# Kernel tuning notes

Hardware: AMD Instinct MI355X
Metric: run time of the kernel (lower is better)

Reference implementation:

```python
import jax, jax.numpy as jnp
import numpy as np

N_NODES = 50000
ALPHA = 0.1
K_ITERS = 10


def setup_inputs() -> dict:
    key = jax.random.key(0)
    ks = jax.random.split(key, 6)
    x = jax.random.normal(ks[0], (N_NODES, 256), dtype=jnp.float32)
    edge_index = jax.random.randint(ks[1], (2, 800000), 0, N_NODES, dtype=jnp.int64)
    # Glorot-ish scaled weights
    W1 = jax.random.normal(ks[2], (256, 128), dtype=jnp.float32) * (1.0 / np.sqrt(256))
    b1 = jnp.zeros((128,), dtype=jnp.float32)
    W3 = jax.random.normal(ks[3], (128, 64), dtype=jnp.float32) * (1.0 / np.sqrt(128))
    b3 = jnp.zeros((64,), dtype=jnp.float32)
    return {"x": x, "edge_index": edge_index, "W1": W1, "b1": b1, "W3": W3, "b3": b3}


def _gcn_norm(edge_index, n_nodes):
    # Add self-loops, then symmetric normalization D^{-1/2} (A+I) D^{-1/2}
    loops = jnp.arange(n_nodes, dtype=edge_index.dtype)
    src = jnp.concatenate([edge_index[0], loops])
    dst = jnp.concatenate([edge_index[1], loops])
    deg = jax.ops.segment_sum(jnp.ones_like(dst, dtype=jnp.float32), dst,
                              num_segments=n_nodes)
    dinv = jnp.where(deg > 0, jax.lax.rsqrt(deg), 0.0)
    w = dinv[src] * dinv[dst]  # [E + N]
    return src, dst, w


def _propagate(h, src, dst, w, n_nodes):
    # out[dst] += w * h[src]  (gather -> scale -> scatter-add)
    msgs = w[:, None] * h[src]
    return jax.ops.segment_sum(msgs, dst, num_segments=n_nodes)


def reference(x, edge_index, W1, b1, W3, b3):
    n = x.shape[0]
    src, dst, w = _gcn_norm(edge_index, n)

    # GCNConv 1: linear then normalized propagation
    h = _propagate(x @ W1 + b1, src, dst, w, n)

    # APPNP: K iterations of h = (1-alpha)*A_hat h + alpha*h0 (eval: no edge dropout)
    h0 = h

    def step(hc, _):
        hn = (1.0 - ALPHA) * _propagate(hc, src, dst, w, n) + ALPHA * h0
        return hn, None

    h, _ = jax.lax.scan(step, h, None, length=K_ITERS)

    # GCNConv 2
    out = _propagate(h @ W3 + b3, src, dst, w, n)
    return out
```

## Files before the change

### kernel.cpp

```cpp
#include <hip/hip_runtime.h>

#define NN 50000
#define NE 800000
#define NT (NE + NN)


__global__ void zero_deg_kernel(int* deg) {
  int v = blockIdx.x * 256 + threadIdx.x;
  if (v < NN) deg[v] = 0;
}

__global__ void count_deg_kernel(const int* __restrict__ edst, int* __restrict__ deg) {
  int i = blockIdx.x * 256 + threadIdx.x;
  if (i < NE) atomicAdd(&deg[edst[i]], 1);
}

__global__ void dinv_kernel(const int* __restrict__ deg, float* __restrict__ dinv) {
  int v = blockIdx.x * 256 + threadIdx.x;
  if (v < NN) dinv[v] = rsqrtf((float)(deg[v] + 1));
}

__global__ __launch_bounds__(1024) void scan1_kernel(const int* __restrict__ deg,
                                                     int* __restrict__ incl,
                                                     int* __restrict__ bsum) {
  __shared__ int sd[1024];
  int gid = blockIdx.x * 1024 + threadIdx.x;
  int v = (gid < NN) ? (deg[gid] + 1) : 0;
  sd[threadIdx.x] = v;
  __syncthreads();
  for (int off = 1; off < 1024; off <<= 1) {
    int t = (threadIdx.x >= off) ? sd[threadIdx.x - off] : 0;
    __syncthreads();
    sd[threadIdx.x] += t;
    __syncthreads();
  }
  if (gid < NN) incl[gid] = sd[threadIdx.x];
  if (threadIdx.x == 1023) bsum[blockIdx.x] = sd[1023];
}

__global__ void scan2_kernel(int* bsum, int nb) {
  if (threadIdx.x == 0 && blockIdx.x == 0) {
    int run = 0;
    for (int i = 0; i < nb; ++i) { int t = bsum[i]; bsum[i] = run; run += t; }
  }
}

__global__ void scan3_kernel(const int* __restrict__ deg, const int* __restrict__ incl,
                             const int* __restrict__ bsum, int* __restrict__ offs,
                             int* __restrict__ cursor) {
  int v = blockIdx.x * 256 + threadIdx.x;
  if (v >= NN) return;
  int o = bsum[v >> 10] + incl[v] - (deg[v] + 1);
  offs[v] = o;
  cursor[v] = o;
  if (v == 0) offs[NN] = NT;
}

__global__ void fill_kernel(const int* __restrict__ esrc, const int* __restrict__ edst,
                            const float* __restrict__ dinv, int* __restrict__ cursor,
                            int2* __restrict__ edges) {
  int i = blockIdx.x * 256 + threadIdx.x;
  if (i >= NT) return;
  int s, d;
  if (i < NE) { s = esrc[i]; d = edst[i]; }
  else        { s = d = i - NE; }
  int p = atomicAdd(&cursor[d], 1);
  int2 e;
  e.x = s;
  e.y = __float_as_int(dinv[s] * dinv[d]);
  edges[p] = e;
}

__global__ void rowsum_kernel(const int* __restrict__ offs, const int2* __restrict__ edges,
                              float* __restrict__ rowsum) {
  int v = blockIdx.x * 256 + threadIdx.x;
  if (v >= NN) return;
  float s = 0.f;
  int e1 = offs[v + 1];
  for (int e = offs[v]; e < e1; ++e) s += __int_as_float(edges[e].y);
  rowsum[v] = s;
}


__global__ void w13_kernel(const float* __restrict__ W1, const float* __restrict__ W3,
                           float* __restrict__ W13) {
  int idx = blockIdx.x * 256 + threadIdx.x;
  if (idx >= 256 * 64) return;
  int r = idx >> 6, c = idx & 63;
  float acc = 0.f;
  for (int k = 0; k < 128; ++k) acc += W1[r * 128 + k] * W3[k * 64 + c];
  W13[idx] = acc;
}

__global__ void b13_kernel(const float* __restrict__ b1, const float* __restrict__ W3,
                           float* __restrict__ b13) {
  int c = threadIdx.x;
  if (c >= 64) return;
  float acc = 0.f;
  for (int k = 0; k < 128; ++k) acc += b1[k] * W3[k * 64 + c];
  b13[c] = acc;
}


template <int K>
__global__ __launch_bounds__(256) void gemm64_kernel(const float* __restrict__ A,
                                                     const float* __restrict__ W,
                                                     const float* __restrict__ bias,
                                                     float* __restrict__ out, int M) {
  __shared__ float xs[32][33];
  __shared__ float ws[32][64];

  int tid = threadIdx.x;
  int tc = tid >> 4;
  int tr = tid & 15;
  int row0 = blockIdx.x * 32;

  float acc[2][4] = {};

  for (int kc = 0; kc < K; kc += 32) {
    {
      int r = tid >> 3, k4 = tid & 7;
      int row = row0 + r;
      float4 v = make_float4(0.f, 0.f, 0.f, 0.f);
      if (row < M) v = *reinterpret_cast<const float4*>(&A[(size_t)row * K + kc + k4 * 4]);
      xs[r][k4 * 4 + 0] = v.x;
      xs[r][k4 * 4 + 1] = v.y;
      xs[r][k4 * 4 + 2] = v.z;
      xs[r][k4 * 4 + 3] = v.w;
    }
    for (int i = tid; i < 512; i += 256) {
      int k = i >> 4, c4 = i & 15;
      *reinterpret_cast<float4*>(&ws[k][c4 * 4]) =
          *reinterpret_cast<const float4*>(&W[(size_t)(kc + k) * 64 + c4 * 4]);
    }
    __syncthreads();
#pragma unroll
    for (int k = 0; k < 32; ++k) {
      float x0 = xs[tr * 2 + 0][k];
      float x1 = xs[tr * 2 + 1][k];
      float4 wv = *reinterpret_cast<const float4*>(&ws[k][tc * 4]);
      acc[0][0] += x0 * wv.x; acc[0][1] += x0 * wv.y;
      acc[0][2] += x0 * wv.z; acc[0][3] += x0 * wv.w;
      acc[1][0] += x1 * wv.x; acc[1][1] += x1 * wv.y;
      acc[1][2] += x1 * wv.z; acc[1][3] += x1 * wv.w;
    }
    __syncthreads();
  }

  float4 bv = *reinterpret_cast<const float4*>(&bias[tc * 4]);
#pragma unroll
  for (int r = 0; r < 2; ++r) {
    int row = row0 + tr * 2 + r;
    if (row < M) {
      float4 o;
      o.x = acc[r][0] + bv.x;
      o.y = acc[r][1] + bv.y;
      o.z = acc[r][2] + bv.z;
      o.w = acc[r][3] + bv.w;
      *reinterpret_cast<float4*>(&out[(size_t)row * 64 + tc * 4]) = o;
    }
  }
}


template <int MODE>
__global__ __launch_bounds__(256) void prop64_kernel(const float* __restrict__ hin,
                                                     const float* __restrict__ h0,
                                                     float* __restrict__ out,
                                                     const int* __restrict__ offs,
                                                     const int2* __restrict__ edges,
                                                     const float* __restrict__ rowsum,
                                                     const float* __restrict__ b3) {
  int node = blockIdx.x * 16 + (threadIdx.x >> 4);
  if (node >= NN) return;
  int f = (threadIdx.x & 15) * 4;
  const float* __restrict__ hb = hin + f;

  int e = offs[node];
  int e1 = offs[node + 1];
  float ax = 0.f, ay = 0.f, az = 0.f, aw = 0.f;

  for (; e + 7 < e1; e += 8) {
    int2 m[8];
#pragma unroll
    for (int j = 0; j < 8; ++j) m[j] = edges[e + j];
    float4 v[8];
#pragma unroll
    for (int j = 0; j < 8; ++j)
      v[j] = *reinterpret_cast<const float4*>(hb + (size_t)m[j].x * 64);
#pragma unroll
    for (int j = 0; j < 8; ++j) {
      float wv = __int_as_float(m[j].y);
      ax += wv * v[j].x; ay += wv * v[j].y; az += wv * v[j].z; aw += wv * v[j].w;
    }
  }
  for (; e + 1 < e1; e += 2) {
    int2 m0 = edges[e], m1 = edges[e + 1];
    float4 v0 = *reinterpret_cast<const float4*>(hb + (size_t)m0.x * 64);
    float4 v1 = *reinterpret_cast<const float4*>(hb + (size_t)m1.x * 64);
    float w0 = __int_as_float(m0.y), w1 = __int_as_float(m1.y);
    ax += w0 * v0.x + w1 * v1.x;
    ay += w0 * v0.y + w1 * v1.y;
    az += w0 * v0.z + w1 * v1.z;
    aw += w0 * v0.w + w1 * v1.w;
  }
  if (e < e1) {
    int2 m = edges[e];
    float4 v = *reinterpret_cast<const float4*>(hb + (size_t)m.x * 64);
    float wv = __int_as_float(m.y);
    ax += wv * v.x; ay += wv * v.y; az += wv * v.z; aw += wv * v.w;
  }

  if (MODE == 1) {
    float4 z = *reinterpret_cast<const float4*>(&h0[(size_t)node * 64 + f]);
    ax = 0.9f * ax + 0.1f * z.x;
    ay = 0.9f * ay + 0.1f * z.y;
    az = 0.9f * az + 0.1f * z.z;
    aw = 0.9f * aw + 0.1f * z.w;
  }
  if (MODE == 2) {
    float rs = rowsum[node];
    float4 bz = *reinterpret_cast<const float4*>(&b3[f]);
    ax += rs * bz.x; ay += rs * bz.y; az += rs * bz.z; aw += rs * bz.w;
  }
  float4 o = make_float4(ax, ay, az, aw);
  *reinterpret_cast<float4*>(&out[(size_t)node * 64 + f]) = o;
}


extern "C" void kernel_launch(void* const* d_in, const int* in_sizes, int n_in,
                              void* d_out, int out_size, void* d_ws, size_t ws_size,
                              hipStream_t stream) {
  const float* x    = (const float*)d_in[0];
  const int*   eidx = (const int*)d_in[1];
  const float* W1   = (const float*)d_in[2];
  const float* b1   = (const float*)d_in[3];
  const float* W3   = (const float*)d_in[4];
  const float* b3   = (const float*)d_in[5];
  float* outp = (float*)d_out;

  const int* esrc = eidx;
  const int* edst = eidx + NE;

  char* w = (char*)d_ws;
  size_t off = 0;
  auto take = [&](size_t bytes) {
    void* p = w + off;
    off = (off + bytes + 255) & ~(size_t)255;
    return p;
  };
  int*   deg    = (int*)take(NN * 4);
  float* dinv   = (float*)take(NN * 4);
  int*   incl   = (int*)take(NN * 4);
  int*   offs   = (int*)take((NN + 1) * 4);
  int*   cursor = (int*)take(NN * 4);
  int*   bsum   = (int*)take(64 * 4);
  float* rsum   = (float*)take(NN * 4);
  float* W13    = (float*)take(256 * 64 * 4);
  float* b13    = (float*)take(64 * 4);
  int2*  edges  = (int2*)take((size_t)NT * 8);
  float* y0     = (float*)take((size_t)NN * 64 * 4);
  float* z0     = (float*)take((size_t)NN * 64 * 4);
  float* zp     = (float*)take((size_t)NN * 64 * 4);
  float* zq     = (float*)take((size_t)NN * 64 * 4);
  (void)ws_size; (void)in_sizes; (void)n_in; (void)out_size;

  const int nblkN = (NN + 255) / 256;
  const int nblkE = (NE + 255) / 256;
  const int nblkT = (NT + 255) / 256;
  const int nbScan = (NN + 1023) / 1024;

  w13_kernel<<<64, 256, 0, stream>>>(W1, W3, W13);
  b13_kernel<<<1, 64, 0, stream>>>(b1, W3, b13);

  zero_deg_kernel<<<nblkN, 256, 0, stream>>>(deg);
  count_deg_kernel<<<nblkE, 256, 0, stream>>>(edst, deg);
  dinv_kernel<<<nblkN, 256, 0, stream>>>(deg, dinv);
  scan1_kernel<<<nbScan, 1024, 0, stream>>>(deg, incl, bsum);
  scan2_kernel<<<1, 64, 0, stream>>>(bsum, nbScan);
  scan3_kernel<<<nblkN, 256, 0, stream>>>(deg, incl, bsum, offs, cursor);
  fill_kernel<<<nblkT, 256, 0, stream>>>(esrc, edst, dinv, cursor, edges);
  rowsum_kernel<<<nblkN, 256, 0, stream>>>(offs, edges, rsum);

  gemm64_kernel<256><<<(NN + 31) / 32, 256, 0, stream>>>(x, W13, b13, y0, NN);

  const int pblk = (NN + 15) / 16;

  prop64_kernel<0><<<pblk, 256, 0, stream>>>(y0, nullptr, z0, offs, edges, nullptr, nullptr);

  const float* hc = z0;
  float* bufs[2] = {zp, zq};
  for (int it = 0; it < 10; ++it) {
    float* hn = bufs[it & 1];
    prop64_kernel<1><<<pblk, 256, 0, stream>>>(hc, z0, hn, offs, edges, nullptr, nullptr);
    hc = hn;
  }

  prop64_kernel<2><<<pblk, 256, 0, stream>>>(hc, nullptr, outp, offs, edges, rsum, b3);
}
```

Before: 515.4 us.

## Pad CSR rows to multiples of 8, split SoA edges, degree-sort nodes, retile GEMM

Each CSR row is padded to a multiple of 8 with zero-weight entries, and edge sources and weights move into separate arrays. This lets the propagation loop do aligned int4/float4 loads in one branch-free 8-wide loop. Nodes are bucketed by padded degree into a permutation, so the 16 nodes in a block have similar trip counts and wave divergence drops. The GEMM tile grows to 64 rows with 4x4 register blocking and vector LDS reads. The cost is more preprocessing kernels and extra padded traffic, since padded edges still gather h[0].

```diff
diff --git a/kernel.cpp b/kernel.cpp
--- a/kernel.cpp
+++ b/kernel.cpp
@@ -2,12 +2,13 @@
 
 #define NN 50000
 #define NE 800000
-#define NT (NE + NN)
-
-
-__global__ void zero_deg_kernel(int* deg) {
+#define NTP (NE + 8 * NN)
+
+
+__global__ void zero_deg_kernel(int* deg, int* hist) {
   int v = blockIdx.x * 256 + threadIdx.x;
   if (v < NN) deg[v] = 0;
+  if (v < 16) hist[v] = 0;
 }
 
 __global__ void count_deg_kernel(const int* __restrict__ edst, int* __restrict__ deg) {
@@ -18,6 +19,10 @@
 __global__ void dinv_kernel(const int* __restrict__ deg, float* __restrict__ dinv) {
   int v = blockIdx.x * 256 + threadIdx.x;
   if (v < NN) dinv[v] = rsqrtf((float)(deg[v] + 1));
+}
+
+__device__ __forceinline__ int pdeg_of(int deg) {
+  return ((deg + 8) >> 3) << 3;
 }
 
 __global__ __launch_bounds__(1024) void scan1_kernel(const int* __restrict__ deg,
@@ -25,7 +30,7 @@
                                                      int* __restrict__ bsum) {
   __shared__ int sd[1024];
   int gid = blockIdx.x * 1024 + threadIdx.x;
-  int v = (gid < NN) ? (deg[gid] + 1) : 0;
+  int v = (gid < NN) ? pdeg_of(deg[gid]) : 0;
   sd[threadIdx.x] = v;
   __syncthreads();
   for (int off = 1; off < 1024; off <<= 1) {
@@ -50,35 +55,71 @@
                              int* __restrict__ cursor) {
   int v = blockIdx.x * 256 + threadIdx.x;
   if (v >= NN) return;
-  int o = bsum[v >> 10] + incl[v] - (deg[v] + 1);
+  int pd = pdeg_of(deg[v]);
+  int o = bsum[v >> 10] + incl[v] - pd;
   offs[v] = o;
   cursor[v] = o;
-  if (v == 0) offs[NN] = NT;
+  if (v == NN - 1) offs[NN] = o + pd;
+}
+
+__global__ void zero_csrc_kernel(int* csrc) {
+  int i = blockIdx.x * 256 + threadIdx.x;
+  if (i < NTP) csrc[i] = 0;
 }
 
 __global__ void fill_kernel(const int* __restrict__ esrc, const int* __restrict__ edst,
-                            const float* __restrict__ dinv, int* __restrict__ cursor,
-                            int2* __restrict__ edges) {
+                            int* __restrict__ cursor, int* __restrict__ csrc) {
   int i = blockIdx.x * 256 + threadIdx.x;
-  if (i >= NT) return;
+  if (i >= NE + NN) return;
   int s, d;
   if (i < NE) { s = esrc[i]; d = edst[i]; }
   else        { s = d = i - NE; }
   int p = atomicAdd(&cursor[d], 1);
-  int2 e;
-  e.x = s;
-  e.y = __float_as_int(dinv[s] * dinv[d]);
-  edges[p] = e;
-}
-
-__global__ void rowsum_kernel(const int* __restrict__ offs, const int2* __restrict__ edges,
-                              float* __restrict__ rowsum) {
+  csrc[p] = s;
+}
+
+__global__ void cwrs_kernel(const int* __restrict__ deg, const float* __restrict__ dinv,
+                            const int* __restrict__ offs, const int* __restrict__ csrc,
+                            float* __restrict__ cw, float* __restrict__ rowsum) {
   int v = blockIdx.x * 256 + threadIdx.x;
   if (v >= NN) return;
+  float dv = dinv[v];
+  int r = deg[v] + 1;
+  int e0 = offs[v], e1 = offs[v + 1];
   float s = 0.f;
-  int e1 = offs[v + 1];
-  for (int e = offs[v]; e < e1; ++e) s += __int_as_float(edges[e].y);
+  for (int e = e0; e < e1; ++e) {
+    int j = e - e0;
+    float w = 0.f;
+    if (j < r) { w = dinv[csrc[e]] * dv; s += w; }
+    cw[e] = w;
+  }
   rowsum[v] = s;
+}
+
+
+__global__ void hist_kernel(const int* __restrict__ deg, int* __restrict__ hist) {
+  int v = blockIdx.x * 256 + threadIdx.x;
+  if (v >= NN) return;
+  int b = pdeg_of(deg[v]) >> 3;
+  if (b > 15) b = 15;
+  atomicAdd(&hist[b], 1);
+}
+
+__global__ void hscan_kernel(const int* __restrict__ hist, int* __restrict__ hcur) {
+  if (threadIdx.x == 0 && blockIdx.x == 0) {
+    int run = 0;
+    for (int i = 0; i < 16; ++i) { hcur[i] = run; run += hist[i]; }
+  }
+}
+
+__global__ void permfill_kernel(const int* __restrict__ deg, int* __restrict__ hcur,
+                                int* __restrict__ perm) {
+  int v = blockIdx.x * 256 + threadIdx.x;
+  if (v >= NN) return;
+  int b = pdeg_of(deg[v]) >> 3;
+  if (b > 15) b = 15;
+  int p = atomicAdd(&hcur[b], 1);
+  perm[p] = v;
 }
 
 
@@ -107,26 +148,23 @@
                                                      const float* __restrict__ W,
                                                      const float* __restrict__ bias,
                                                      float* __restrict__ out, int M) {
-  __shared__ float xs[32][33];
+  __shared__ float xs[64][36];
   __shared__ float ws[32][64];
 
   int tid = threadIdx.x;
-  int tc = tid >> 4;
-  int tr = tid & 15;
-  int row0 = blockIdx.x * 32;
-
-  float acc[2][4] = {};
+  int tc = tid & 15;
+  int tr = tid >> 4;
+  int row0 = blockIdx.x * 64;
+
+  float acc[4][4] = {};
 
   for (int kc = 0; kc < K; kc += 32) {
-    {
-      int r = tid >> 3, k4 = tid & 7;
+    for (int i = tid; i < 512; i += 256) {
+      int r = i >> 3, k4 = i & 7;
       int row = row0 + r;
       float4 v = make_float4(0.f, 0.f, 0.f, 0.f);
       if (row < M) v = *reinterpret_cast<const float4*>(&A[(size_t)row * K + kc + k4 * 4]);
-      xs[r][k4 * 4 + 0] = v.x;
-      xs[r][k4 * 4 + 1] = v.y;
-      xs[r][k4 * 4 + 2] = v.z;
-      xs[r][k4 * 4 + 3] = v.w;
+      *reinterpret_cast<float4*>(&xs[r][k4 * 4]) = v;
     }
     for (int i = tid; i < 512; i += 256) {
       int k = i >> 4, c4 = i & 15;
@@ -135,22 +173,29 @@
     }
     __syncthreads();
 #pragma unroll
-    for (int k = 0; k < 32; ++k) {
-      float x0 = xs[tr * 2 + 0][k];
-      float x1 = xs[tr * 2 + 1][k];
-      float4 wv = *reinterpret_cast<const float4*>(&ws[k][tc * 4]);
-      acc[0][0] += x0 * wv.x; acc[0][1] += x0 * wv.y;
-      acc[0][2] += x0 * wv.z; acc[0][3] += x0 * wv.w;
-      acc[1][0] += x1 * wv.x; acc[1][1] += x1 * wv.y;
-      acc[1][2] += x1 * wv.z; acc[1][3] += x1 * wv.w;
+    for (int kk = 0; kk < 32; kk += 4) {
+      float4 xv[4], wv[4];
+#pragma unroll
+      for (int r = 0; r < 4; ++r)
+        xv[r] = *reinterpret_cast<const float4*>(&xs[tr * 4 + r][kk]);
+#pragma unroll
+      for (int q = 0; q < 4; ++q)
+        wv[q] = *reinterpret_cast<const float4*>(&ws[kk + q][tc * 4]);
+#pragma unroll
+      for (int r = 0; r < 4; ++r) {
+        acc[r][0] += xv[r].x * wv[0].x + xv[r].y * wv[1].x + xv[r].z * wv[2].x + xv[r].w * wv[3].x;
+        acc[r][1] += xv[r].x * wv[0].y + xv[r].y * wv[1].y + xv[r].z * wv[2].y + xv[r].w * wv[3].y;
+        acc[r][2] += xv[r].x * wv[0].z + xv[r].y * wv[1].z + xv[r].z * wv[2].z + xv[r].w * wv[3].z;
+        acc[r][3] += xv[r].x * wv[0].w + xv[r].y * wv[1].w + xv[r].z * wv[2].w + xv[r].w * wv[3].w;
+      }
     }
     __syncthreads();
   }
 
   float4 bv = *reinterpret_cast<const float4*>(&bias[tc * 4]);
 #pragma unroll
-  for (int r = 0; r < 2; ++r) {
-    int row = row0 + tr * 2 + r;
+  for (int r = 0; r < 4; ++r) {
+    int row = row0 + tr * 4 + r;
     if (row < M) {
       float4 o;
       o.x = acc[r][0] + bv.x;
@@ -168,11 +213,14 @@
                                                      const float* __restrict__ h0,
                                                      float* __restrict__ out,
                                                      const int* __restrict__ offs,
-                                                     const int2* __restrict__ edges,
+                                                     const int* __restrict__ csrc,
+                                                     const float* __restrict__ cw,
+                                                     const int* __restrict__ perm,
                                                      const float* __restrict__ rowsum,
                                                      const float* __restrict__ b3) {
-  int node = blockIdx.x * 16 + (threadIdx.x >> 4);
-  if (node >= NN) return;
+  int gi = blockIdx.x * 16 + (threadIdx.x >> 4);
+  if (gi >= NN) return;
+  int node = perm[gi];
   int f = (threadIdx.x & 15) * 4;
   const float* __restrict__ hb = hin + f;
 
@@ -180,35 +228,27 @@
   int e1 = offs[node + 1];
   float ax = 0.f, ay = 0.f, az = 0.f, aw = 0.f;
 
-  for (; e + 7 < e1; e += 8) {
-    int2 m[8];
-#pragma unroll
-    for (int j = 0; j < 8; ++j) m[j] = edges[e + j];
-    float4 v[8];
-#pragma unroll
-    for (int j = 0; j < 8; ++j)
-      v[j] = *reinterpret_cast<const float4*>(hb + (size_t)m[j].x * 64);
-#pragma unroll
-    for (int j = 0; j < 8; ++j) {
-      float wv = __int_as_float(m[j].y);
-      ax += wv * v[j].x; ay += wv * v[j].y; az += wv * v[j].z; aw += wv * v[j].w;
-    }
-  }
-  for (; e + 1 < e1; e += 2) {
-    int2 m0 = edges[e], m1 = edges[e + 1];
-    float4 v0 = *reinterpret_cast<const float4*>(hb + (size_t)m0.x * 64);
-    float4 v1 = *reinterpret_cast<const float4*>(hb + (size_t)m1.x * 64);
-    float w0 = __int_as_float(m0.y), w1 = __int_as_float(m1.y);
-    ax += w0 * v0.x + w1 * v1.x;
-    ay += w0 * v0.y + w1 * v1.y;
-    az += w0 * v0.z + w1 * v1.z;
-    aw += w0 * v0.w + w1 * v1.w;
-  }
-  if (e < e1) {
-    int2 m = edges[e];
-    float4 v = *reinterpret_cast<const float4*>(hb + (size_t)m.x * 64);
-    float wv = __int_as_float(m.y);
-    ax += wv * v.x; ay += wv * v.y; az += wv * v.z; aw += wv * v.w;
+  for (; e < e1; e += 8) {
+    int4 sa = *reinterpret_cast<const int4*>(csrc + e);
+    int4 sb = *reinterpret_cast<const int4*>(csrc + e + 4);
+    float4 wa = *reinterpret_cast<const float4*>(cw + e);
+    float4 wb = *reinterpret_cast<const float4*>(cw + e + 4);
+    float4 v0 = *reinterpret_cast<const float4*>(hb + (size_t)sa.x * 64);
+    float4 v1 = *reinterpret_cast<const float4*>(hb + (size_t)sa.y * 64);
+    float4 v2 = *reinterpret_cast<const float4*>(hb + (size_t)sa.z * 64);
+    float4 v3 = *reinterpret_cast<const float4*>(hb + (size_t)sa.w * 64);
+    float4 v4 = *reinterpret_cast<const float4*>(hb + (size_t)sb.x * 64);
+    float4 v5 = *reinterpret_cast<const float4*>(hb + (size_t)sb.y * 64);
+    float4 v6 = *reinterpret_cast<const float4*>(hb + (size_t)sb.z * 64);
+    float4 v7 = *reinterpret_cast<const float4*>(hb + (size_t)sb.w * 64);
+    ax += wa.x * v0.x + wa.y * v1.x + wa.z * v2.x + wa.w * v3.x
+        + wb.x * v4.x + wb.y * v5.x + wb.z * v6.x + wb.w * v7.x;
+    ay += wa.x * v0.y + wa.y * v1.y + wa.z * v2.y + wa.w * v3.y
+        + wb.x * v4.y + wb.y * v5.y + wb.z * v6.y + wb.w * v7.y;
+    az += wa.x * v0.z + wa.y * v1.z + wa.z * v2.z + wa.w * v3.z
+        + wb.x * v4.z + wb.y * v5.z + wb.z * v6.z + wb.w * v7.z;
+    aw += wa.x * v0.w + wa.y * v1.w + wa.z * v2.w + wa.w * v3.w
+        + wb.x * v4.w + wb.y * v5.w + wb.z * v6.w + wb.w * v7.w;
   }
 
   if (MODE == 1) {
@@ -255,10 +295,14 @@
   int*   offs   = (int*)take((NN + 1) * 4);
   int*   cursor = (int*)take(NN * 4);
   int*   bsum   = (int*)take(64 * 4);
+  int*   hist   = (int*)take(16 * 4);
+  int*   hcur   = (int*)take(16 * 4);
+  int*   perm   = (int*)take(NN * 4);
   float* rsum   = (float*)take(NN * 4);
   float* W13    = (float*)take(256 * 64 * 4);
   float* b13    = (float*)take(64 * 4);
-  int2*  edges  = (int2*)take((size_t)NT * 8);
+  int*   csrc   = (int*)take((size_t)NTP * 4);
+  float* cw     = (float*)take((size_t)NTP * 4);
   float* y0     = (float*)take((size_t)NN * 64 * 4);
   float* z0     = (float*)take((size_t)NN * 64 * 4);
   float* zp     = (float*)take((size_t)NN * 64 * 4);
@@ -267,34 +311,40 @@
 
   const int nblkN = (NN + 255) / 256;
   const int nblkE = (NE + 255) / 256;
-  const int nblkT = (NT + 255) / 256;
+  const int nblkF = (NE + NN + 255) / 256;
+  const int nblkP = (NTP + 255) / 256;
   const int nbScan = (NN + 1023) / 1024;
 
   w13_kernel<<<64, 256, 0, stream>>>(W1, W3, W13);
   b13_kernel<<<1, 64, 0, stream>>>(b1, W3, b13);
 
-  zero_deg_kernel<<<nblkN, 256, 0, stream>>>(deg);
+  zero_deg_kernel<<<nblkN, 256, 0, stream>>>(deg, hist);
   count_deg_kernel<<<nblkE, 256, 0, stream>>>(edst, deg);
   dinv_kernel<<<nblkN, 256, 0, stream>>>(deg, dinv);
   scan1_kernel<<<nbScan, 1024, 0, stream>>>(deg, incl, bsum);
   scan2_kernel<<<1, 64, 0, stream>>>(bsum, nbScan);
   scan3_kernel<<<nblkN, 256, 0, stream>>>(deg, incl, bsum, offs, cursor);
-  fill_kernel<<<nblkT, 256, 0, stream>>>(esrc, edst, dinv, cursor, edges);
-  rowsum_kernel<<<nblkN, 256, 0, stream>>>(offs, edges, rsum);
-
-  gemm64_kernel<256><<<(NN + 31) / 32, 256, 0, stream>>>(x, W13, b13, y0, NN);
+  zero_csrc_kernel<<<nblkP, 256, 0, stream>>>(csrc);
+  fill_kernel<<<nblkF, 256, 0, stream>>>(esrc, edst, cursor, csrc);
+  cwrs_kernel<<<nblkN, 256, 0, stream>>>(deg, dinv, offs, csrc, cw, rsum);
+
+  hist_kernel<<<nblkN, 256, 0, stream>>>(deg, hist);
+  hscan_kernel<<<1, 64, 0, stream>>>(hist, hcur);
+  permfill_kernel<<<nblkN, 256, 0, stream>>>(deg, hcur, perm);
+
+  gemm64_kernel<256><<<(NN + 63) / 64, 256, 0, stream>>>(x, W13, b13, y0, NN);
 
   const int pblk = (NN + 15) / 16;
 
-  prop64_kernel<0><<<pblk, 256, 0, stream>>>(y0, nullptr, z0, offs, edges, nullptr, nullptr);
+  prop64_kernel<0><<<pblk, 256, 0, stream>>>(y0, nullptr, z0, offs, csrc, cw, perm, nullptr, nullptr);
 
   const float* hc = z0;
   float* bufs[2] = {zp, zq};
   for (int it = 0; it < 10; ++it) {
     float* hn = bufs[it & 1];
-    prop64_kernel<1><<<pblk, 256, 0, stream>>>(hc, z0, hn, offs, edges, nullptr, nullptr);
+    prop64_kernel<1><<<pblk, 256, 0, stream>>>(hc, z0, hn, offs, csrc, cw, perm, nullptr, nullptr);
     hc = hn;
   }
 
-  prop64_kernel<2><<<pblk, 256, 0, stream>>>(hc, nullptr, outp, offs, edges, rsum, b3);
-}
+  prop64_kernel<2><<<pblk, 256, 0, stream>>>(hc, nullptr, outp, offs, csrc, cw, perm, rsum, b3);
+}
```

Result: slower. 1.304 ms (+152.9%).

## Pad CSR rows to multiples of eight and enlarge GEMM register tile

Applied to the files above, without the earlier changes.

Each node's CSR row length (degree plus self-loop) is rounded up to a multiple of eight, and the padding slots are zeroed as (src 0, weight 0) entries. The propagation loop then always processes full groups of eight, with 16-byte vector loads for the edge records and no remainder loops. The GEMM is also retiled to 64 rows per block with a 4x4 register tile and float4 shared-memory reads. Padding adds wasted gathers of node 0 plus an extra zeroing kernel, in exchange for branch-free, vectorised inner loops.

```diff
diff --git a/kernel.cpp b/kernel.cpp
--- a/kernel.cpp
+++ b/kernel.cpp
@@ -2,7 +2,7 @@
 
 #define NN 50000
 #define NE 800000
-#define NT (NE + NN)
+#define NTP (NE + 8 * NN)
 
 
 __global__ void zero_deg_kernel(int* deg) {
@@ -18,6 +18,10 @@
 __global__ void dinv_kernel(const int* __restrict__ deg, float* __restrict__ dinv) {
   int v = blockIdx.x * 256 + threadIdx.x;
   if (v < NN) dinv[v] = rsqrtf((float)(deg[v] + 1));
+}
+
+__device__ __forceinline__ int pdeg_of(int deg) {
+  return ((deg + 8) >> 3) << 3;
 }
 
 __global__ __launch_bounds__(1024) void scan1_kernel(const int* __restrict__ deg,
@@ -25,7 +29,7 @@
                                                      int* __restrict__ bsum) {
   __shared__ int sd[1024];
   int gid = blockIdx.x * 1024 + threadIdx.x;
-  int v = (gid < NN) ? (deg[gid] + 1) : 0;
+  int v = (gid < NN) ? pdeg_of(deg[gid]) : 0;
   sd[threadIdx.x] = v;
   __syncthreads();
   for (int off = 1; off < 1024; off <<= 1) {
@@ -50,17 +54,23 @@
                              int* __restrict__ cursor) {
   int v = blockIdx.x * 256 + threadIdx.x;
   if (v >= NN) return;
-  int o = bsum[v >> 10] + incl[v] - (deg[v] + 1);
+  int pd = pdeg_of(deg[v]);
+  int o = bsum[v >> 10] + incl[v] - pd;
   offs[v] = o;
   cursor[v] = o;
-  if (v == 0) offs[NN] = NT;
+  if (v == NN - 1) offs[NN] = o + pd;
+}
+
+__global__ void zero_edges_kernel(int2* edges) {
+  int i = blockIdx.x * 256 + threadIdx.x;
+  if (i < NTP) edges[i] = make_int2(0, 0);
 }
 
 __global__ void fill_kernel(const int* __restrict__ esrc, const int* __restrict__ edst,
                             const float* __restrict__ dinv, int* __restrict__ cursor,
                             int2* __restrict__ edges) {
   int i = blockIdx.x * 256 + threadIdx.x;
-  if (i >= NT) return;
+  if (i >= NE + NN) return;
   int s, d;
   if (i < NE) { s = esrc[i]; d = edst[i]; }
   else        { s = d = i - NE; }
@@ -107,26 +117,23 @@
                                                      const float* __restrict__ W,
                                                      const float* __restrict__ bias,
                                                      float* __restrict__ out, int M) {
-  __shared__ float xs[32][33];
+  __shared__ float xs[64][36];
   __shared__ float ws[32][64];
 
   int tid = threadIdx.x;
-  int tc = tid >> 4;
-  int tr = tid & 15;
-  int row0 = blockIdx.x * 32;
-
-  float acc[2][4] = {};
+  int tc = tid & 15;
+  int tr = tid >> 4;
+  int row0 = blockIdx.x * 64;
+
+  float acc[4][4] = {};
 
   for (int kc = 0; kc < K; kc += 32) {
-    {
-      int r = tid >> 3, k4 = tid & 7;
+    for (int i = tid; i < 512; i += 256) {
+      int r = i >> 3, k4 = i & 7;
       int row = row0 + r;
       float4 v = make_float4(0.f, 0.f, 0.f, 0.f);
       if (row < M) v = *reinterpret_cast<const float4*>(&A[(size_t)row * K + kc + k4 * 4]);
-      xs[r][k4 * 4 + 0] = v.x;
-      xs[r][k4 * 4 + 1] = v.y;
-      xs[r][k4 * 4 + 2] = v.z;
-      xs[r][k4 * 4 + 3] = v.w;
+      *reinterpret_cast<float4*>(&xs[r][k4 * 4]) = v;
     }
     for (int i = tid; i < 512; i += 256) {
       int k = i >> 4, c4 = i & 15;
@@ -135,22 +142,29 @@
     }
     __syncthreads();
 #pragma unroll
-    for (int k = 0; k < 32; ++k) {
-      float x0 = xs[tr * 2 + 0][k];
-      float x1 = xs[tr * 2 + 1][k];
-      float4 wv = *reinterpret_cast<const float4*>(&ws[k][tc * 4]);
-      acc[0][0] += x0 * wv.x; acc[0][1] += x0 * wv.y;
-      acc[0][2] += x0 * wv.z; acc[0][3] += x0 * wv.w;
-      acc[1][0] += x1 * wv.x; acc[1][1] += x1 * wv.y;
-      acc[1][2] += x1 * wv.z; acc[1][3] += x1 * wv.w;
+    for (int kk = 0; kk < 32; kk += 4) {
+      float4 xv[4], wv[4];
+#pragma unroll
+      for (int r = 0; r < 4; ++r)
+        xv[r] = *reinterpret_cast<const float4*>(&xs[tr * 4 + r][kk]);
+#pragma unroll
+      for (int q = 0; q < 4; ++q)
+        wv[q] = *reinterpret_cast<const float4*>(&ws[kk + q][tc * 4]);
+#pragma unroll
+      for (int r = 0; r < 4; ++r) {
+        acc[r][0] += xv[r].x * wv[0].x + xv[r].y * wv[1].x + xv[r].z * wv[2].x + xv[r].w * wv[3].x;
+        acc[r][1] += xv[r].x * wv[0].y + xv[r].y * wv[1].y + xv[r].z * wv[2].y + xv[r].w * wv[3].y;
+        acc[r][2] += xv[r].x * wv[0].z + xv[r].y * wv[1].z + xv[r].z * wv[2].z + xv[r].w * wv[3].z;
+        acc[r][3] += xv[r].x * wv[0].w + xv[r].y * wv[1].w + xv[r].z * wv[2].w + xv[r].w * wv[3].w;
+      }
     }
     __syncthreads();
   }
 
   float4 bv = *reinterpret_cast<const float4*>(&bias[tc * 4]);
 #pragma unroll
-  for (int r = 0; r < 2; ++r) {
-    int row = row0 + tr * 2 + r;
+  for (int r = 0; r < 4; ++r) {
+    int row = row0 + tr * 4 + r;
     if (row < M) {
       float4 o;
       o.x = acc[r][0] + bv.x;
@@ -180,35 +194,31 @@
   int e1 = offs[node + 1];
   float ax = 0.f, ay = 0.f, az = 0.f, aw = 0.f;
 
-  for (; e + 7 < e1; e += 8) {
-    int2 m[8];
-#pragma unroll
-    for (int j = 0; j < 8; ++j) m[j] = edges[e + j];
-    float4 v[8];
-#pragma unroll
-    for (int j = 0; j < 8; ++j)
-      v[j] = *reinterpret_cast<const float4*>(hb + (size_t)m[j].x * 64);
-#pragma unroll
-    for (int j = 0; j < 8; ++j) {
-      float wv = __int_as_float(m[j].y);
-      ax += wv * v[j].x; ay += wv * v[j].y; az += wv * v[j].z; aw += wv * v[j].w;
-    }
-  }
-  for (; e + 1 < e1; e += 2) {
-    int2 m0 = edges[e], m1 = edges[e + 1];
-    float4 v0 = *reinterpret_cast<const float4*>(hb + (size_t)m0.x * 64);
-    float4 v1 = *reinterpret_cast<const float4*>(hb + (size_t)m1.x * 64);
-    float w0 = __int_as_float(m0.y), w1 = __int_as_float(m1.y);
-    ax += w0 * v0.x + w1 * v1.x;
-    ay += w0 * v0.y + w1 * v1.y;
-    az += w0 * v0.z + w1 * v1.z;
-    aw += w0 * v0.w + w1 * v1.w;
-  }
-  if (e < e1) {
-    int2 m = edges[e];
-    float4 v = *reinterpret_cast<const float4*>(hb + (size_t)m.x * 64);
-    float wv = __int_as_float(m.y);
-    ax += wv * v.x; ay += wv * v.y; az += wv * v.z; aw += wv * v.w;
+  for (; e < e1; e += 8) {
+    int4 m01 = *reinterpret_cast<const int4*>(edges + e);
+    int4 m23 = *reinterpret_cast<const int4*>(edges + e + 2);
+    int4 m45 = *reinterpret_cast<const int4*>(edges + e + 4);
+    int4 m67 = *reinterpret_cast<const int4*>(edges + e + 6);
+    float4 v0 = *reinterpret_cast<const float4*>(hb + (size_t)m01.x * 64);
+    float4 v1 = *reinterpret_cast<const float4*>(hb + (size_t)m01.z * 64);
+    float4 v2 = *reinterpret_cast<const float4*>(hb + (size_t)m23.x * 64);
+    float4 v3 = *reinterpret_cast<const float4*>(hb + (size_t)m23.z * 64);
+    float4 v4 = *reinterpret_cast<const float4*>(hb + (size_t)m45.x * 64);
+    float4 v5 = *reinterpret_cast<const float4*>(hb + (size_t)m45.z * 64);
+    float4 v6 = *reinterpret_cast<const float4*>(hb + (size_t)m67.x * 64);
+    float4 v7 = *reinterpret_cast<const float4*>(hb + (size_t)m67.z * 64);
+    float w0 = __int_as_float(m01.y), w1 = __int_as_float(m01.w);
+    float w2 = __int_as_float(m23.y), w3 = __int_as_float(m23.w);
+    float w4 = __int_as_float(m45.y), w5 = __int_as_float(m45.w);
+    float w6 = __int_as_float(m67.y), w7 = __int_as_float(m67.w);
+    ax += w0 * v0.x + w1 * v1.x + w2 * v2.x + w3 * v3.x
+        + w4 * v4.x + w5 * v5.x + w6 * v6.x + w7 * v7.x;
+    ay += w0 * v0.y + w1 * v1.y + w2 * v2.y + w3 * v3.y
+        + w4 * v4.y + w5 * v5.y + w6 * v6.y + w7 * v7.y;
+    az += w0 * v0.z + w1 * v1.z + w2 * v2.z + w3 * v3.z
+        + w4 * v4.z + w5 * v5.z + w6 * v6.z + w7 * v7.z;
+    aw += w0 * v0.w + w1 * v1.w + w2 * v2.w + w3 * v3.w
+        + w4 * v4.w + w5 * v5.w + w6 * v6.w + w7 * v7.w;
   }
 
   if (MODE == 1) {
@@ -258,7 +268,7 @@
   float* rsum   = (float*)take(NN * 4);
   float* W13    = (float*)take(256 * 64 * 4);
   float* b13    = (float*)take(64 * 4);
-  int2*  edges  = (int2*)take((size_t)NT * 8);
+  int2*  edges  = (int2*)take((size_t)NTP * 8);
   float* y0     = (float*)take((size_t)NN * 64 * 4);
   float* z0     = (float*)take((size_t)NN * 64 * 4);
   float* zp     = (float*)take((size_t)NN * 64 * 4);
@@ -267,7 +277,8 @@
 
   const int nblkN = (NN + 255) / 256;
   const int nblkE = (NE + 255) / 256;
-  const int nblkT = (NT + 255) / 256;
+  const int nblkF = (NE + NN + 255) / 256;
+  const int nblkP = (NTP + 255) / 256;
   const int nbScan = (NN + 1023) / 1024;
 
   w13_kernel<<<64, 256, 0, stream>>>(W1, W3, W13);
@@ -279,10 +290,11 @@
   scan1_kernel<<<nbScan, 1024, 0, stream>>>(deg, incl, bsum);
   scan2_kernel<<<1, 64, 0, stream>>>(bsum, nbScan);
   scan3_kernel<<<nblkN, 256, 0, stream>>>(deg, incl, bsum, offs, cursor);
-  fill_kernel<<<nblkT, 256, 0, stream>>>(esrc, edst, dinv, cursor, edges);
+  zero_edges_kernel<<<nblkP, 256, 0, stream>>>(edges);
+  fill_kernel<<<nblkF, 256, 0, stream>>>(esrc, edst, dinv, cursor, edges);
   rowsum_kernel<<<nblkN, 256, 0, stream>>>(offs, edges, rsum);
 
-  gemm64_kernel<256><<<(NN + 31) / 32, 256, 0, stream>>>(x, W13, b13, y0, NN);
+  gemm64_kernel<256><<<(NN + 63) / 64, 256, 0, stream>>>(x, W13, b13, y0, NN);
 
   const int pblk = (NN + 15) / 16;
 
```

Result: no change. 512.8 us (-0.5%).
